# Kernel optimization log

Hardware: AMD Instinct MI355X
Metric: run time of the kernel (lower is better)

The kernel has to match this reference:

```python
import jax, jax.numpy as jnp
import numpy as np

NH, NKV, HD = 16, 4, 128
ROPE_THETA = 10000.0


def setup_inputs() -> dict:
    key = jax.random.key(0)
    ks = jax.random.split(key, 5)
    std = jnp.float32(0.02)
    return {
        "hidden_states": jax.random.normal(ks[0], (1, 2048, 2048), jnp.float32),
        "wq": jax.random.normal(ks[1], (2048, NH * HD), jnp.float32) * std,
        "wk": jax.random.normal(ks[2], (2048, NKV * HD), jnp.float32) * std,
        "wv": jax.random.normal(ks[3], (2048, NKV * HD), jnp.float32) * std,
        "wo": jax.random.normal(ks[4], (NH * HD, 2048), jnp.float32) * std,
    }


def _rope(x, cos, sin):
    # x: [B,S,n,hd]; pairs (even,odd) treated as complex, multiplied by cis(angle)
    xr = x.reshape(*x.shape[:-1], HD // 2, 2)
    re, im = xr[..., 0], xr[..., 1]
    c = cos[None, :, None, :]  # [1,S,1,hd/2]
    s = sin[None, :, None, :]
    out = jnp.stack((re * c - im * s, re * s + im * c), axis=-1)
    return out.reshape(x.shape)


def reference(hidden_states, wq, wk, wv, wo):
    B, S, H = hidden_states.shape
    q = (hidden_states @ wq).reshape(B, S, NH, HD)
    k = (hidden_states @ wk).reshape(B, S, NKV, HD)
    v = (hidden_states @ wv).reshape(B, S, NKV, HD)

    # precompute_freqs_cis (full rotary dim, rot_dim=None)
    freqs = 1.0 / (ROPE_THETA ** (jnp.arange(0, HD, 2, dtype=jnp.float32) / HD))
    ang = jnp.outer(jnp.arange(S, dtype=jnp.float32), freqs)  # [S, hd/2]
    cos, sin = jnp.cos(ang), jnp.sin(ang)

    q = _rope(q.astype(jnp.float32), cos, sin)
    k = _rope(k.astype(jnp.float32), cos, sin)

    # GQA: repeat_kv == repeat_interleave over head axis
    n_rep = NH // NKV
    k = jnp.repeat(k, n_rep, axis=2)  # [B,S,NH,HD]
    v = jnp.repeat(v, n_rep, axis=2)

    scale = jnp.float32(1.0 / np.sqrt(HD))
    scores = jnp.einsum("bqhd,bkhd->bhqk", q, k) * scale
    causal = jnp.tril(jnp.ones((S, S), dtype=bool))
    scores = jnp.where(causal[None, None], scores, jnp.float32(-1e9))
    attn = jax.nn.softmax(scores, axis=-1)
    out = jnp.einsum("bhqk,bkhd->bqhd", attn, v).reshape(B, S, NH * HD)
    return out @ wo
```

## Files before the change

### kernel.cpp

```cpp
#include <hip/hip_runtime.h>
#include <cstdint>

typedef __attribute__((ext_vector_type(8))) short short8;
typedef __attribute__((ext_vector_type(4))) float f32x4;

static __device__ __forceinline__ unsigned short f2bf(float x) {
  union { float f; unsigned int u; } c; c.f = x;
  unsigned int u = c.u;
  unsigned int r = (u + 0x7fffu + ((u >> 16) & 1u)) >> 16;
  return (unsigned short)r;
}

static __device__ __forceinline__ unsigned int cvt_pk_bf16(float a, float b) {
  unsigned int r;
  asm("v_cvt_pk_bf16_f32 %0, %1, %2" : "=v"(r) : "v"(a), "v"(b));
  return r;
}

static __device__ __forceinline__ void gl_lds16(const void* g, void* l) {
  __builtin_amdgcn_global_load_lds((const __attribute__((address_space(1))) void*)g,
                                   (__attribute__((address_space(3))) void*)l, 16, 0, 0);
}

__global__ __launch_bounds__(256) void k_prep(const float* __restrict__ wq,
                                              const float* __restrict__ wk,
                                              const float* __restrict__ wv,
                                              const float* __restrict__ wo,
                                              const float* __restrict__ hs,
                                              unsigned short* __restrict__ wqt,
                                              unsigned short* __restrict__ wkt,
                                              unsigned short* __restrict__ wvt,
                                              unsigned short* __restrict__ wot,
                                              unsigned short* __restrict__ hb,
                                              float2* __restrict__ ctab) {
  int id = blockIdx.x;
  if (id >= 10240) {
    if (id < 14336) {
      int i = (id - 10240) * 256 + threadIdx.x;
      float4 v = reinterpret_cast<const float4*>(hs)[i];
      ushort4 o;
      o.x = f2bf(v.x); o.y = f2bf(v.y); o.z = f2bf(v.z); o.w = f2bf(v.w);
      reinterpret_cast<ushort4*>(hb)[i] = o;
    } else {
      int idx = (id - 14336) * 256 + threadIdx.x;
      int s = idx >> 6, i = idx & 63;
      float freq = powf(10000.0f, -(float)i / 64.0f);
      float sn, cs;
      sincosf((float)s * freq, &sn, &cs);
      ctab[idx] = make_float2(cs, sn);
    }
    return;
  }
  __shared__ float tile[32][33];
  const float* src; unsigned short* dst; int N, t;
  if (id < 4096)       { src = wq; dst = wqt; N = 2048; t = id; }
  else if (id < 8192)  { src = wo; dst = wot; N = 2048; t = id - 4096; }
  else if (id < 9216)  { src = wk; dst = wkt; N = 512;  t = id - 8192; }
  else                 { src = wv; dst = wvt; N = 512;  t = id - 9216; }
  const int K = 2048;
  int ntx = N >> 5;
  int bn = (t % ntx) * 32, bk = (t / ntx) * 32;
  int tx = threadIdx.x & 31, ty = threadIdx.x >> 5;
#pragma unroll
  for (int i = 0; i < 32; i += 8)
    tile[ty + i][tx] = src[(size_t)(bk + ty + i) * N + bn + tx];
  __syncthreads();
#pragma unroll
  for (int i = 0; i < 32; i += 8)
    dst[(size_t)(bn + ty + i) * K + bk + tx] = f2bf(tile[tx][ty + i]);
}

__global__ __launch_bounds__(256) void k_gemm_bf16(const unsigned short* __restrict__ A,
                                                   const unsigned short* __restrict__ Bt,
                                                   float* __restrict__ C,
                                                   unsigned short* __restrict__ Qd,
                                                   unsigned short* __restrict__ Kd,
                                                   unsigned short* __restrict__ VT,
                                                   const float2* __restrict__ ctab,
                                                   int M, int N, int K, int fuse) {
  __shared__ short sA[2][128 * 64];
  __shared__ short sB[2][64 * 64];
  int tid = threadIdx.x;
  int lane = tid & 63, wid = tid >> 6;
  int wr = wid >> 1, wc = wid & 1;

  int gx = gridDim.x, nwg = gx * gridDim.y;
  int flat = blockIdx.y * gx + blockIdx.x;
  int l = (flat & 7) * (nwg >> 3) + (flat >> 3);
  int bx = l % gx, by = l / gx;
  int m0 = by * 128, n0 = bx * 64;

  f32x4 acc[4][2] = {};

  int srcCol = (((tid & 7) ^ ((tid >> 3) & 7)) << 3);
  int rA = tid >> 3;
  const unsigned short* Ag = A + (size_t)(m0 + rA) * K + srcCol;
  const unsigned short* Bg = Bt + (size_t)(n0 + rA) * K + srcCol;
  int wb = (tid & ~63) * 8;

  int g = lane >> 4, fr = lane & 15, sw = fr & 7;

#define STAGE_G(buf, kof) do { \
    gl_lds16(Ag + (kof),                    &sA[buf][wb]); \
    gl_lds16(Ag + 32 * (size_t)K + (kof),   &sA[buf][2048 + wb]); \
    gl_lds16(Ag + 64 * (size_t)K + (kof),   &sA[buf][4096 + wb]); \
    gl_lds16(Ag + 96 * (size_t)K + (kof),   &sA[buf][6144 + wb]); \
    gl_lds16(Bg + (kof),                    &sB[buf][wb]); \
    gl_lds16(Bg + 32 * (size_t)K + (kof),   &sB[buf][2048 + wb]); \
  } while (0)

  int nt = K >> 6;
  STAGE_G(0, 0);
  __syncthreads();

  int cur = 0;
  for (int t = 0; t < nt; t++) {
    if (t + 1 < nt) STAGE_G(cur ^ 1, (size_t)((t + 1) << 6));
    const short* sAc = sA[cur];
    const short* sBc = sB[cur];
#pragma unroll
    for (int kk = 0; kk < 2; kk++) {
      int so = ((((kk << 2) + g) ^ sw) << 3);
      short8 af[4], bf2[2];
#pragma unroll
      for (int x = 0; x < 4; x++)
        af[x] = *(const short8*)(sAc + (wr * 64 + x * 16 + fr) * 64 + so);
#pragma unroll
      for (int ni = 0; ni < 2; ni++)
        bf2[ni] = *(const short8*)(sBc + (wc * 32 + ni * 16 + fr) * 64 + so);
#pragma unroll
      for (int x = 0; x < 4; x++)
#pragma unroll
        for (int ni = 0; ni < 2; ni++)
          acc[x][ni] = __builtin_amdgcn_mfma_f32_16x16x32_bf16(af[x], bf2[ni], acc[x][ni], 0, 0, 0);
    }
    __syncthreads();
    cur ^= 1;
  }
#undef STAGE_G

  int rb = m0 + wr * 64 + (g << 2);
  if (!fuse) {
#pragma unroll
    for (int ni = 0; ni < 2; ni++) {
      int col = n0 + wc * 32 + ni * 16 + fr;
#pragma unroll
      for (int x = 0; x < 4; x++)
#pragma unroll
        for (int j = 0; j < 4; j++)
          C[(size_t)(rb + x * 16 + j) * N + col] = acc[x][ni][j];
    }
    return;
  }

  const float QAMP = 0.12751742836257666f;
#pragma unroll
  for (int ni = 0; ni < 2; ni++) {
    int col = n0 + wc * 32 + ni * 16 + fr;
    if (col >= 2560) {
#pragma unroll
      for (int x = 0; x < 4; x++) {
        ushort4 pk;
        pk.x = f2bf(acc[x][ni][0]); pk.y = f2bf(acc[x][ni][1]);
        pk.z = f2bf(acc[x][ni][2]); pk.w = f2bf(acc[x][ni][3]);
        *(ushort4*)(VT + (size_t)(col - 2560) * 2048 + rb + x * 16) = pk;
      }
    } else {
      int ipair = (col & 127) >> 1;
      bool even = (col & 1) == 0;
      bool isQ = col < 2048;
      unsigned short* dst = isQ ? Qd : Kd;
      int stride = isQ ? 2048 : 512;
      int dcol = isQ ? col : (col - 2048);
      float amp = isQ ? QAMP : 1.0f;
#pragma unroll
      for (int x = 0; x < 4; x++) {
        f32x4 a = acc[x][ni];
        float p0 = __shfl_xor(a[0], 1), p1 = __shfl_xor(a[1], 1);
        float p2 = __shfl_xor(a[2], 1), p3 = __shfl_xor(a[3], 1);
        float pv[4] = {p0, p1, p2, p3};
#pragma unroll
        for (int j = 0; j < 4; j++) {
          int r = rb + x * 16 + j;
          float2 cs = ctab[r * 64 + ipair];
          float o = even ? (a[j] * cs.x - pv[j] * cs.y)
                         : (pv[j] * cs.y + a[j] * cs.x);
          dst[(size_t)r * stride + dcol] = f2bf(o * amp);
        }
      }
    }
  }
}

#define KSTR 136
#define VSTR 72
#define PSTR 72
__global__ __launch_bounds__(512) void k_attn_mfma(const unsigned short* __restrict__ Qb,
                                                   const unsigned short* __restrict__ Kb,
                                                   const unsigned short* __restrict__ Vt,
                                                   unsigned short* __restrict__ O) {
  __shared__ short sK[2][64 * KSTR];
  __shared__ short sV[2][128 * VSTR];
  __shared__ short sP[8][16 * PSTR];
  int b = blockIdx.x;
  int qb = 31 - (b >> 4);
  int h = b & 15;
  int q0 = qb * 64;
  int kvh = h >> 2;
  int tid = threadIdx.x, lane = tid & 63, w8 = tid >> 6;
  int g4 = w8 & 3;
  int p = w8 >> 2;
  int fr = lane & 15, g = lane >> 4, kq = g << 3;

  short8 qf[4];
  {
    const unsigned short* qrow = Qb + (size_t)(q0 + g4 * 16 + fr) * 2048 + h * 128 + kq;
#pragma unroll
    for (int ko = 0; ko < 4; ko++) qf[ko] = *(const short8*)(qrow + ko * 32);
  }

  f32x4 oacc[8];
#pragma unroll
  for (int nd = 0; nd < 8; nd++) oacc[nd] = (f32x4){0.f, 0.f, 0.f, 0.f};
  float m_i = -3e38f;
  float l_i = 0.f;

  int half = tid >> 8;
  int t2 = tid & 255;
  int skr = t2 >> 2, skc = (t2 & 3) << 5;
  int svd = t2 >> 1, svc = (t2 & 1) << 5;
  const unsigned short* Kbase = Kb + (size_t)kvh * 128 + skc;
  const unsigned short* Vbase = Vt + (size_t)(kvh * 128 + svd) * 2048 + svc;
  short* pw = (short*)sP[w8];
  int kdOff = skr * KSTR + skc;
  int vdOff = svd * VSTR + svc;

  short8 kreg[4], vreg[4];
  if (half <= qb) {
    const short8* ks = (const short8*)(Kbase + (size_t)(half * 64 + skr) * 512);
    const short8* vs = (const short8*)(Vbase + half * 64);
#pragma unroll
    for (int j = 0; j < 4; j++) { kreg[j] = ks[j]; vreg[j] = vs[j]; }
    short* kd = sK[half] + kdOff; short* vd = sV[half] + vdOff;
#pragma unroll
    for (int j = 0; j < 4; j++) { *(short8*)(kd + j * 8) = kreg[j]; *(short8*)(vd + j * 8) = vreg[j]; }
  }
  if (2 + half <= qb) {
    const short8* ks = (const short8*)(Kbase + (size_t)((2 + half) * 64 + skr) * 512);
    const short8* vs = (const short8*)(Vbase + (2 + half) * 64);
#pragma unroll
    for (int j = 0; j < 4; j++) { kreg[j] = ks[j]; vreg[j] = vs[j]; }
  }
  __syncthreads();

  int qrowS = q0 + g4 * 16 + fr;
  int nIter = (qb + 2) >> 1;

  for (int i = 0; i < nIter; i++) {
    int t = 2 * i + p;
    if (t <= qb) {
      const short* sKc = sK[p];
      const short* sVc = sV[p];

      f32x4 sacc[4];
#pragma unroll
      for (int ni = 0; ni < 4; ni++) sacc[ni] = (f32x4){0.f, 0.f, 0.f, 0.f};
      __builtin_amdgcn_s_setprio(1);
#pragma unroll
      for (int ko = 0; ko < 4; ko++)
#pragma unroll
        for (int ni = 0; ni < 4; ni++) {
          short8 kf = *(const short8*)(sKc + (ni * 16 + fr) * KSTR + kq + ko * 32);
          sacc[ni] = __builtin_amdgcn_mfma_f32_16x16x32_bf16(kf, qf[ko], sacc[ni], 0, 0, 0);
        }
      __builtin_amdgcn_s_setprio(0);

      if (t == qb) {
        int k0 = t * 64;
#pragma unroll
        for (int ni = 0; ni < 4; ni++) {
          int kc = k0 + ni * 16 + (g << 2);
#pragma unroll
          for (int j = 0; j < 4; j++)
            if (kc + j > qrowS) sacc[ni][j] = -3e38f;
        }
      }

      float t0m = fmaxf(fmaxf(sacc[0][0], sacc[0][1]), fmaxf(sacc[0][2], sacc[0][3]));
      float t1m = fmaxf(fmaxf(sacc[1][0], sacc[1][1]), fmaxf(sacc[1][2], sacc[1][3]));
      float t2m = fmaxf(fmaxf(sacc[2][0], sacc[2][1]), fmaxf(sacc[2][2], sacc[2][3]));
      float t3m = fmaxf(fmaxf(sacc[3][0], sacc[3][1]), fmaxf(sacc[3][2], sacc[3][3]));
      float tm = fmaxf(fmaxf(t0m, t1m), fmaxf(t2m, t3m));
      tm = fmaxf(tm, __shfl_xor(tm, 16));
      tm = fmaxf(tm, __shfl_xor(tm, 32));

      if (!__all(tm <= m_i + 8.0f)) {
        float mn = fmaxf(m_i, tm);
        float sc = exp2f(m_i - mn);
        m_i = mn;
        float scj[4];
#pragma unroll
        for (int j = 0; j < 4; j++) scj[j] = __shfl(sc, (g << 2) + j);
#pragma unroll
        for (int nd = 0; nd < 8; nd++)
#pragma unroll
          for (int j = 0; j < 4; j++) oacc[nd][j] *= scj[j];
        l_i *= sc;
      }

      float ps = 0.f;
#pragma unroll
      for (int ni = 0; ni < 4; ni++) {
        float p0 = exp2f(sacc[ni][0] - m_i);
        float p1 = exp2f(sacc[ni][1] - m_i);
        float p2 = exp2f(sacc[ni][2] - m_i);
        float p3 = exp2f(sacc[ni][3] - m_i);
        ps += (p0 + p1) + (p2 + p3);
        uint2 pk;
        pk.x = cvt_pk_bf16(p0, p1);
        pk.y = cvt_pk_bf16(p2, p3);
        *(uint2*)(pw + fr * PSTR + ni * 16 + (g << 2)) = pk;
      }
      ps += __shfl_xor(ps, 16);
      ps += __shfl_xor(ps, 32);
      l_i += ps;

      __builtin_amdgcn_s_setprio(1);
#pragma unroll
      for (int ks = 0; ks < 2; ks++) {
        short8 pa = *(const short8*)(pw + fr * PSTR + kq + ks * 32);
#pragma unroll
        for (int nd = 0; nd < 8; nd++) {
          short8 vb = *(const short8*)(sVc + (nd * 16 + fr) * VSTR + kq + ks * 32);
          oacc[nd] = __builtin_amdgcn_mfma_f32_16x16x32_bf16(pa, vb, oacc[nd], 0, 0, 0);
        }
      }
      __builtin_amdgcn_s_setprio(0);
    }

    if (i + 1 < nIter) {
      __syncthreads();
      int tn = 2 * (i + 1) + half;
      if (tn <= qb) {
        short* kd = sK[half] + kdOff; short* vd = sV[half] + vdOff;
#pragma unroll
        for (int j = 0; j < 4; j++) { *(short8*)(kd + j * 8) = kreg[j]; *(short8*)(vd + j * 8) = vreg[j]; }
      }
      int tl = 2 * (i + 2) + half;
      if (tl <= qb) {
        const short8* ks = (const short8*)(Kbase + (size_t)(tl * 64 + skr) * 512);
        const short8* vs = (const short8*)(Vbase + tl * 64);
#pragma unroll
        for (int j = 0; j < 4; j++) { kreg[j] = ks[j]; vreg[j] = vs[j]; }
      }
      __syncthreads();
    }
  }

  __syncthreads();
  float* onum = (float*)sK;
  float* mlb = (float*)sV;
  if (p == 1) {
    int r0 = g4 * 16;
#pragma unroll
    for (int j = 0; j < 4; j++)
#pragma unroll
      for (int nd = 0; nd < 8; nd++)
        onum[(r0 + (g << 2) + j) * 128 + nd * 16 + fr] = oacc[nd][j];
    if (g == 0) {
      mlb[(r0 + fr) * 2] = m_i;
      mlb[(r0 + fr) * 2 + 1] = l_i;
    }
  }
  __syncthreads();
  if (p == 0) {
    int orow = q0 + g4 * 16 + (g << 2);
    int r0 = g4 * 16;
#pragma unroll
    for (int j = 0; j < 4; j++) {
      int rl = (g << 2) + j;
      float ma = __shfl(m_i, rl);
      float la = __shfl(l_i, rl);
      float mb = mlb[(r0 + rl) * 2];
      float lb = mlb[(r0 + rl) * 2 + 1];
      float M = fmaxf(ma, mb);
      float wa = exp2f(ma - M), wbv = exp2f(mb - M);
      float inv = 1.0f / (wa * la + wbv * lb);
#pragma unroll
      for (int nd = 0; nd < 8; nd++) {
        float ob = onum[(r0 + rl) * 128 + nd * 16 + fr];
        O[(size_t)(orow + j) * 2048 + h * 128 + nd * 16 + fr] =
            f2bf((wa * oacc[nd][j] + wbv * ob) * inv);
      }
    }
  }
}

extern "C" void kernel_launch(void* const* d_in, const int* in_sizes, int n_in,
                              void* d_out, int out_size, void* d_ws, size_t ws_size,
                              hipStream_t stream) {
  const float* hs = (const float*)d_in[0];
  const float* wq = (const float*)d_in[1];
  const float* wk = (const float*)d_in[2];
  const float* wv = (const float*)d_in[3];
  const float* wo = (const float*)d_in[4];
  char* ws = (char*)d_ws;

  unsigned short* hb   = (unsigned short*)(ws);
  unsigned short* wqt  = (unsigned short*)(ws + 8388608);
  unsigned short* wkt  = (unsigned short*)(ws + 16777216);
  unsigned short* wvt  = (unsigned short*)(ws + 18874368);
  unsigned short* wot  = (unsigned short*)(ws + 20971520);
  unsigned short* q_bf = (unsigned short*)(ws + 29360128);
  unsigned short* k_bf = (unsigned short*)(ws + 37748736);
  unsigned short* vt_bf= (unsigned short*)(ws + 39845888);
  float2* ctab         = (float2*)(ws + 41943040);
  unsigned short* ao   = hb;
  float* out = (float*)d_out;

  k_prep<<<14848, 256, 0, stream>>>(wq, wk, wv, wo, hs, wqt, wkt, wvt, wot, hb, ctab);

  k_gemm_bf16<<<dim3(48, 16), 256, 0, stream>>>(hb, wqt, (float*)nullptr,
                                                q_bf, k_bf, vt_bf, ctab,
                                                2048, 3072, 2048, 1);

  k_attn_mfma<<<512, 512, 0, stream>>>(q_bf, k_bf, vt_bf, ao);

  k_gemm_bf16<<<dim3(32, 16), 256, 0, stream>>>(ao, wot, out,
                                                (unsigned short*)nullptr,
                                                (unsigned short*)nullptr,
                                                (unsigned short*)nullptr,
                                                (const float2*)nullptr,
                                                2048, 2048, 2048, 0);
}
```

Before: 136.6 us.

## Redistribute P via lane shuffles instead of LDS and rebalance attention grid

The softmax probability tile, previously written to a per-wave shared-memory scratch and read back in MFMA A-operand layout, is now rearranged in registers using cross-lane shuffles and selects. This removes the sP LDS buffer and its write/read round trip, freeing shared memory, at the cost of eight 32-bit shuffles per k-step. The launch grid also changes to 2D (32 x 16) with half the heads walking query blocks in ascending order and half in descending order, which changes the scheduling order of the uneven causal workloads.

```diff
diff --git a/kernel.cpp b/kernel.cpp
--- a/kernel.cpp
+++ b/kernel.cpp
@@ -14,6 +14,13 @@
 static __device__ __forceinline__ unsigned int cvt_pk_bf16(float a, float b) {
   unsigned int r;
   asm("v_cvt_pk_bf16_f32 %0, %1, %2" : "=v"(r) : "v"(a), "v"(b));
+  return r;
+}
+
+static __device__ __forceinline__ uint2 shfl64(uint2 v, int lane) {
+  uint2 r;
+  r.x = (unsigned int)__shfl((int)v.x, lane);
+  r.y = (unsigned int)__shfl((int)v.y, lane);
   return r;
 }
 
@@ -194,17 +201,15 @@
 
 #define KSTR 136
 #define VSTR 72
-#define PSTR 72
 __global__ __launch_bounds__(512) void k_attn_mfma(const unsigned short* __restrict__ Qb,
                                                    const unsigned short* __restrict__ Kb,
                                                    const unsigned short* __restrict__ Vt,
                                                    unsigned short* __restrict__ O) {
   __shared__ short sK[2][64 * KSTR];
   __shared__ short sV[2][128 * VSTR];
-  __shared__ short sP[8][16 * PSTR];
-  int b = blockIdx.x;
-  int qb = 31 - (b >> 4);
-  int h = b & 15;
+  int h = blockIdx.y;
+  int x = blockIdx.x;
+  int qb = (h < 8) ? x : (31 - x);
   int q0 = qb * 64;
   int kvh = h >> 2;
   int tid = threadIdx.x, lane = tid & 63, w8 = tid >> 6;
@@ -231,7 +236,6 @@
   int svd = t2 >> 1, svc = (t2 & 1) << 5;
   const unsigned short* Kbase = Kb + (size_t)kvh * 128 + skc;
   const unsigned short* Vbase = Vt + (size_t)(kvh * 128 + svd) * 2048 + svc;
-  short* pw = (short*)sP[w8];
   int kdOff = skr * KSTR + skc;
   int vdOff = svd * VSTR + svc;
 
@@ -255,6 +259,10 @@
 
   int qrowS = q0 + g4 * 16 + fr;
   int nIter = (qb + 2) >> 1;
+
+  int srcA = fr + ((g & 1) << 5);
+  int srcB = srcA + 16;
+  int rsel = g >> 1;
 
   for (int i = 0; i < nIter; i++) {
     int t = 2 * i + p;
@@ -308,6 +316,7 @@
         l_i *= sc;
       }
 
+      uint2 Pk[4];
       float ps = 0.f;
 #pragma unroll
       for (int ni = 0; ni < 4; ni++) {
@@ -316,10 +325,8 @@
         float p2 = exp2f(sacc[ni][2] - m_i);
         float p3 = exp2f(sacc[ni][3] - m_i);
         ps += (p0 + p1) + (p2 + p3);
-        uint2 pk;
-        pk.x = cvt_pk_bf16(p0, p1);
-        pk.y = cvt_pk_bf16(p2, p3);
-        *(uint2*)(pw + fr * PSTR + ni * 16 + (g << 2)) = pk;
+        Pk[ni].x = cvt_pk_bf16(p0, p1);
+        Pk[ni].y = cvt_pk_bf16(p2, p3);
       }
       ps += __shfl_xor(ps, 16);
       ps += __shfl_xor(ps, 32);
@@ -328,7 +335,16 @@
       __builtin_amdgcn_s_setprio(1);
 #pragma unroll
       for (int ks = 0; ks < 2; ks++) {
-        short8 pa = *(const short8*)(pw + fr * PSTR + kq + ks * 32);
+        uint2 A0 = shfl64(Pk[2 * ks],     srcA);
+        uint2 A1 = shfl64(Pk[2 * ks + 1], srcA);
+        uint2 B0 = shfl64(Pk[2 * ks],     srcB);
+        uint2 B1 = shfl64(Pk[2 * ks + 1], srcB);
+        union { unsigned int u[4]; short8 s; } pc;
+        pc.u[0] = rsel ? A1.x : A0.x;
+        pc.u[1] = rsel ? A1.y : A0.y;
+        pc.u[2] = rsel ? B1.x : B0.x;
+        pc.u[3] = rsel ? B1.y : B0.y;
+        short8 pa = pc.s;
 #pragma unroll
         for (int nd = 0; nd < 8; nd++) {
           short8 vb = *(const short8*)(sVc + (nd * 16 + fr) * VSTR + kq + ks * 32);
@@ -424,7 +440,7 @@
                                                 q_bf, k_bf, vt_bf, ctab,
                                                 2048, 3072, 2048, 1);
 
-  k_attn_mfma<<<512, 512, 0, stream>>>(q_bf, k_bf, vt_bf, ao);
+  k_attn_mfma<<<dim3(32, 16), 512, 0, stream>>>(q_bf, k_bf, vt_bf, ao);
 
   k_gemm_bf16<<<dim3(32, 16), 256, 0, stream>>>(ao, wot, out,
                                                 (unsigned short*)nullptr,
```

Measured after the change: 170.0 us. 24.4% more time.
